# Performance work log

Hardware: AMD Instinct MI355X
Metric: run time of the kernel (lower is better)

Reference implementation:

```python
import jax, jax.numpy as jnp
import numpy as np

B, S, H, N_IN, N_PROC, R = 4, 1024, 1024, 64, 16, 128

def setup_inputs() -> dict:
    key = jax.random.key(0)
    k0, k1, k2, k3, k4 = jax.random.split(key, 5)
    intermediate = jax.random.normal(k0, (B, S, H), dtype=jnp.float32)
    enriched_activations = jax.random.normal(k1, (B, S, N_IN), dtype=jnp.float32)
    # Conv2d(1 -> N_proc, kernel=(5, N_in)), default PyTorch init scale ~ 1/sqrt(fan_in)
    fan_in = 1 * 5 * N_IN
    conv_w = jax.random.uniform(k2, (N_PROC, 1, 5, N_IN), dtype=jnp.float32,
                                minval=-1.0, maxval=1.0) / np.sqrt(fan_in).astype(np.float32)
    conv_b = jnp.zeros((N_PROC,), dtype=jnp.float32)
    down_proj = 0.02 * jax.random.normal(k3, (N_PROC, H, R), dtype=jnp.float32)
    up_proj = 0.02 * jax.random.normal(k4, (N_PROC, R, H), dtype=jnp.float32)
    return {"intermediate": intermediate, "enriched_activations": enriched_activations,
            "conv_w": conv_w, "conv_b": conv_b, "down_proj": down_proj, "up_proj": up_proj}

def reference(intermediate, enriched_activations, conv_w, conv_b, down_proj, up_proj):
    # act_map: [B, 1, S, N_in]; conv kernel (5, N_in) with padding (2, 0) -> [B, N_proc, S, 1]
    act_map = enriched_activations[:, None, :, :]
    pr = jax.lax.conv_general_dilated(
        act_map, conv_w, window_strides=(1, 1), padding=((2, 2), (0, 0)),
        dimension_numbers=("NCHW", "OIHW", "NCHW"))
    pr = pr + conv_b[None, :, None, None]
    # squeeze width, transpose to [B, S, N_proc], sigmoid gate
    process_activations = jax.nn.sigmoid(jnp.transpose(pr[..., 0], (0, 2, 1)))
    # per-expert low-rank transform
    down = jnp.einsum("bsh,nhr->bsnr", intermediate, down_proj)          # [B,S,N,R]
    transformed = jnp.einsum("bsnr,nrh->bsnh", down, up_proj)            # [B,S,N,H]
    # gate-weighted sum over experts (fuses multiply + sum over n)
    output = jnp.einsum("bsnh,bsn->bsh", transformed, process_activations)
    return (output, process_activations)
```

## Files before the change

### kernel.cpp

```cpp
#include <hip/hip_runtime.h>
#include <hip/hip_fp16.h>

#define T_TOK 4096
#define H_DIM 1024
#define NIN   64
#define NP    16
#define R_DIM 128
#define S_DIM 1024
#define N1    (NP * R_DIM)

typedef _Float16 half8  __attribute__((ext_vector_type(8)));
typedef _Float16 half4v __attribute__((ext_vector_type(4)));
typedef float    floatx16 __attribute__((ext_vector_type(16)));

typedef __attribute__((address_space(3))) unsigned char lds_u8_t;
typedef __attribute__((address_space(1))) unsigned char gbl_u8_t;

__device__ __forceinline__ void g2l16(const void* g, void* l) {
  __builtin_amdgcn_global_load_lds((const gbl_u8_t*)g, (lds_u8_t*)l, 16, 0, 0);
}

template <int GATE, int K, int N>
__global__ __launch_bounds__(256)
void gemm_kernel(const _Float16* __restrict__ A, const _Float16* __restrict__ BT,
                 const float* __restrict__ gv, void* __restrict__ Cv) {
  constexpr int NK = K / 64;
  constexpr int GX = N / 128;
  __shared__ __align__(16) _Float16 smem[4][64 * 128];

  const int tid = threadIdx.x, wave = tid >> 6, lane = tid & 63;
  const int id = blockIdx.x;
  const int xcd = id & 7, s = id >> 3;
  const int byi = s / GX + 4 * xcd;
  const int bxi = s % GX;
  const int m0 = byi * 128, n0 = bxi * 128;
  const int wr = (wave >> 1) * 64, wc = (wave & 1) * 64;
  const int rl = lane >> 4, ql = lane & 15;
  const int r = lane & 31, kh = lane >> 5;

  auto stage = [&](const _Float16* __restrict__ base, int off0, int k0,
                   _Float16* dst) {
    #pragma unroll
    for (int c = 0; c < 4; ++c) {
      const int cc = wave * 4 + c;
      const int lrow = cc * 4 + rl;
      const int cl = ql ^ (lrow & 15);
      const int row = lrow + ((cl >> 3) << 6);
      g2l16(base + (size_t)(off0 + row) * K + k0 + (cl & 7) * 8, dst + cc * 512);
    }
  };

  floatx16 acc[2][2];
  #pragma unroll
  for (int i = 0; i < 2; ++i)
    #pragma unroll
    for (int j = 0; j < 2; ++j) acc[i][j] = (floatx16)0.f;

  _Float16 *cA = smem[0], *nA = smem[1], *cB = smem[2], *nB = smem[3];
  stage(A, m0, 0, cA);
  stage(BT, n0, 0, cB);

  #pragma unroll 2
  for (int k = 0; k < NK; ++k) {
    if (k + 1 < NK) {
      stage(A, m0, (k + 1) * 64, nA);
      stage(BT, n0, (k + 1) * 64, nB);
      __builtin_amdgcn_s_waitcnt(0xF78);
    } else {
      __builtin_amdgcn_s_waitcnt(0xF70);
    }
    __builtin_amdgcn_s_barrier();
    __builtin_amdgcn_sched_barrier(0);
    #pragma unroll
    for (int h = 0; h < 4; ++h) {
      const int pA = (2 * h + kh + ((wave >> 1) << 3)) ^ (r & 15);
      const int pB = (2 * h + kh + ((wave & 1) << 3)) ^ (r & 15);
      half8 af[2], bf[2];
      #pragma unroll
      for (int i = 0; i < 2; ++i)
        af[i] = *reinterpret_cast<const half8*>(&cA[(i * 32 + r) * 128 + pA * 8]);
      #pragma unroll
      for (int j = 0; j < 2; ++j)
        bf[j] = *reinterpret_cast<const half8*>(&cB[(j * 32 + r) * 128 + pB * 8]);
      #pragma unroll
      for (int i = 0; i < 2; ++i)
        #pragma unroll
        for (int j = 0; j < 2; ++j)
          acc[i][j] = __builtin_amdgcn_mfma_f32_32x32x16_f16(af[i], bf[j], acc[i][j], 0, 0, 0);
    }
    __builtin_amdgcn_sched_barrier(0);
    __builtin_amdgcn_s_barrier();
    _Float16* t;
    t = cA; cA = nA; nA = t;
    t = cB; cB = nB; nB = t;
  }

  if (GATE) {
    _Float16* C = (_Float16*)Cv;
    #pragma unroll
    for (int i = 0; i < 2; ++i)
      #pragma unroll
      for (int g4 = 0; g4 < 4; ++g4)
        #pragma unroll
        for (int rr = 0; rr < 4; ++rr) {
          const int rowL = wr + i * 32 + rr + 8 * g4 + 4 * kh;
          const float g = gv[(size_t)(m0 + rowL) * NP + bxi];
          #pragma unroll
          for (int j = 0; j < 2; ++j)
            C[(size_t)(m0 + rowL) * N + n0 + wc + j * 32 + r] =
                (_Float16)(acc[i][j][g4 * 4 + rr] * g);
        }
  } else {
    float* C = (float*)Cv;
    #pragma unroll
    for (int i = 0; i < 2; ++i)
      #pragma unroll
      for (int g4 = 0; g4 < 4; ++g4)
        #pragma unroll
        for (int rr = 0; rr < 4; ++rr) {
          const int rowL = wr + i * 32 + rr + 8 * g4 + 4 * kh;
          #pragma unroll
          for (int j = 0; j < 2; ++j)
            C[(size_t)(m0 + rowL) * N + n0 + wc + j * 32 + r] = acc[i][j][g4 * 4 + rr];
        }
  }
}

__global__ __launch_bounds__(256)
void prep_kernel(const float* __restrict__ enr, const float* __restrict__ cw,
                 const float* __restrict__ cb, const float* __restrict__ inter,
                 const float* __restrict__ dproj, const float* __restrict__ uproj,
                 float* __restrict__ gates, _Float16* __restrict__ Xh,
                 _Float16* __restrict__ BT1, _Float16* __restrict__ UT) {
  __shared__ __align__(16) char smem[25664];
  const int tid = threadIdx.x;
  const int bx = blockIdx.x, nb = gridDim.x;
  {
    const float4* src = (const float4*)inter;
    half4v* dst = (half4v*)Xh;
    for (int i = bx * 256 + tid; i < T_TOK * H_DIM / 4; i += nb * 256) {
      float4 v = src[i];
      half4v o;
      o[0] = (_Float16)v.x; o[1] = (_Float16)v.y; o[2] = (_Float16)v.z; o[3] = (_Float16)v.w;
      dst[i] = o;
    }
  }
  if (bx < 256) {
    float (*sw)[321] = (float (*)[321])smem;
    float (*se)[NIN] = (float (*)[NIN])(smem + 20544);
    const int t0 = bx * 16;
    const int b = t0 >> 10, s0 = t0 & 1023;
    for (int i = tid; i < NP * 320; i += 256) sw[i / 320][i % 320] = cw[i];
    for (int i = tid; i < 20 * NIN; i += 256) {
      int rr = i >> 6, c = i & 63, s = s0 + rr - 2;
      se[rr][c] = (s >= 0 && s < S_DIM) ? enr[((size_t)b * S_DIM + s) * NIN + c] : 0.f;
    }
    __syncthreads();
    const int lt = tid >> 4, n = tid & 15;
    float acc = cb[n];
    #pragma unroll
    for (int dh = 0; dh < 5; ++dh) {
      const float* wrow = &sw[n][dh * 64];
      const float* erow = se[lt + dh];
      #pragma unroll
      for (int j = 0; j < NIN; ++j) acc += erow[j] * wrow[j];
    }
    gates[(size_t)(t0 + lt) * NP + n] = 1.f / (1.f + expf(-acc));
    __syncthreads();
  }
  for (int u = bx; u < 4096; u += nb) {
    const float* src; _Float16* dst; int rows, cols, bxt, byt;
    if (u < 2048) {
      int n = u >> 7, rem = u & 127;
      src = dproj + (size_t)n * H_DIM * R_DIM;
      dst = BT1 + (size_t)n * R_DIM * H_DIM;
      rows = H_DIM; cols = R_DIM; bxt = rem & 3; byt = rem >> 2;
    } else {
      int u2 = u - 2048;
      src = uproj; dst = UT; rows = N1; cols = H_DIM;
      bxt = u2 & 31; byt = u2 >> 5;
    }
    float (*tile)[33] = (float (*)[33])smem;
    const int c0 = bxt * 32, r0 = byt * 32;
    const int tx = tid & 31, ty = tid >> 5;
    #pragma unroll
    for (int k = 0; k < 32; k += 8)
      tile[ty + k][tx] = src[(size_t)(r0 + ty + k) * cols + c0 + tx];
    __syncthreads();
    #pragma unroll
    for (int k = 0; k < 32; k += 8)
      dst[(size_t)(c0 + ty + k) * rows + r0 + tx] = (_Float16)tile[tx][ty + k];
    __syncthreads();
  }
}

extern "C" void kernel_launch(void* const* d_in, const int* in_sizes, int n_in,
                              void* d_out, int out_size, void* d_ws, size_t ws_size,
                              hipStream_t stream) {
  const float* inter = (const float*)d_in[0];
  const float* enr   = (const float*)d_in[1];
  const float* convw = (const float*)d_in[2];
  const float* convb = (const float*)d_in[3];
  const float* dproj = (const float*)d_in[4];
  const float* uproj = (const float*)d_in[5];
  float* out   = (float*)d_out;
  float* gates = out + (size_t)T_TOK * H_DIM;

  _Float16* Xh  = (_Float16*)d_ws;
  _Float16* BT1 = Xh  + (size_t)T_TOK * H_DIM;
  _Float16* UT  = BT1 + (size_t)N1 * H_DIM;
  _Float16* Dsc = UT  + (size_t)H_DIM * N1;

  prep_kernel<<<8448, 256, 0, stream>>>(enr, convw, convb, inter, dproj, uproj,
                                        gates, Xh, BT1, UT);
  gemm_kernel<1, H_DIM, N1>
      <<<(N1 / 128) * (T_TOK / 128), 256, 0, stream>>>(Xh, BT1, gates, (void*)Dsc);
  gemm_kernel<0, N1, H_DIM>
      <<<(H_DIM / 128) * (T_TOK / 128), 256, 0, stream>>>(Dsc, UT, nullptr, (void*)out);
}
```

Measured before the change: 133.1 us.

## Fuse both GEMMs into one launch with per-row-block flag synchronization

Merges the down-projection and up-projection GEMMs into a single kernel of 768 blocks. The first 512 blocks compute gated Dsc tiles and atomically bump a per-row-block counter. The last 256 blocks spin on that counter until all 16 column tiles of their row block are written, then run the second GEMM. This removes a kernel launch boundary and lets the second GEMM start on finished row blocks while the first is still running. It relies on block scheduling order to avoid deadlock, and spinning blocks hold CUs while they wait.

```diff
diff --git a/kernel.cpp b/kernel.cpp
--- a/kernel.cpp
+++ b/kernel.cpp
@@ -21,15 +21,14 @@
 }
 
 template <int GATE, int K, int N>
-__global__ __launch_bounds__(256)
-void gemm_kernel(const _Float16* __restrict__ A, const _Float16* __restrict__ BT,
-                 const float* __restrict__ gv, void* __restrict__ Cv) {
+__device__ __forceinline__
+void gemm_body(_Float16* __restrict__ smem,
+               const _Float16* __restrict__ A, const _Float16* __restrict__ BT,
+               const float* __restrict__ gv, void* __restrict__ Cv,
+               int id, int tid, int* byi_out) {
   constexpr int NK = K / 64;
   constexpr int GX = N / 128;
-  __shared__ __align__(16) _Float16 smem[4][64 * 128];
-
-  const int tid = threadIdx.x, wave = tid >> 6, lane = tid & 63;
-  const int id = blockIdx.x;
+  const int wave = tid >> 6, lane = tid & 63;
   const int xcd = id & 7, s = id >> 3;
   const int byi = s / GX + 4 * xcd;
   const int bxi = s % GX;
@@ -37,6 +36,7 @@
   const int wr = (wave >> 1) * 64, wc = (wave & 1) * 64;
   const int rl = lane >> 4, ql = lane & 15;
   const int r = lane & 31, kh = lane >> 5;
+  *byi_out = byi;
 
   auto stage = [&](const _Float16* __restrict__ base, int off0, int k0,
                    _Float16* dst) {
@@ -56,7 +56,7 @@
     #pragma unroll
     for (int j = 0; j < 2; ++j) acc[i][j] = (floatx16)0.f;
 
-  _Float16 *cA = smem[0], *nA = smem[1], *cB = smem[2], *nB = smem[3];
+  _Float16 *cA = smem, *nA = smem + 8192, *cB = smem + 16384, *nB = smem + 24576;
   stage(A, m0, 0, cA);
   stage(BT, n0, 0, cB);
 
@@ -127,14 +127,51 @@
 }
 
 __global__ __launch_bounds__(256)
+void gemm_fused(const _Float16* __restrict__ Xh, const _Float16* __restrict__ BT1,
+                const _Float16* __restrict__ Dsc_c, _Float16* __restrict__ Dsc,
+                const _Float16* __restrict__ UT, const float* __restrict__ gates,
+                float* __restrict__ out, int* __restrict__ flags) {
+  __shared__ __align__(16) _Float16 smem[4 * 64 * 128];
+  const int tid = threadIdx.x;
+  const int bid = blockIdx.x;
+  int byi;
+  if (bid < 512) {
+    gemm_body<1, H_DIM, N1>(smem, Xh, BT1, gates, (void*)Dsc, bid, tid, &byi);
+    __syncthreads();
+    if (tid == 0) {
+      __threadfence();
+      __hip_atomic_fetch_add(&flags[byi], 1, __ATOMIC_RELEASE,
+                             __HIP_MEMORY_SCOPE_AGENT);
+    }
+  } else {
+    const int id = bid - 512;
+    {
+      const int xcd = id & 7, s = id >> 3;
+      byi = s / (H_DIM / 128) + 4 * xcd;
+    }
+    if (tid == 0) {
+      while (__hip_atomic_load(&flags[byi], __ATOMIC_ACQUIRE,
+                               __HIP_MEMORY_SCOPE_AGENT) < 16)
+        __builtin_amdgcn_s_sleep(8);
+      __threadfence();
+    }
+    __syncthreads();
+    int dummy;
+    gemm_body<0, N1, H_DIM>(smem, Dsc_c, UT, nullptr, (void*)out, id, tid, &dummy);
+  }
+}
+
+__global__ __launch_bounds__(256)
 void prep_kernel(const float* __restrict__ enr, const float* __restrict__ cw,
                  const float* __restrict__ cb, const float* __restrict__ inter,
                  const float* __restrict__ dproj, const float* __restrict__ uproj,
                  float* __restrict__ gates, _Float16* __restrict__ Xh,
-                 _Float16* __restrict__ BT1, _Float16* __restrict__ UT) {
+                 _Float16* __restrict__ BT1, _Float16* __restrict__ UT,
+                 int* __restrict__ flags) {
   __shared__ __align__(16) char smem[25664];
   const int tid = threadIdx.x;
   const int bx = blockIdx.x, nb = gridDim.x;
+  if (bx == 0 && tid < 32) flags[tid] = 0;
   {
     const float4* src = (const float4*)inter;
     half4v* dst = (half4v*)Xh;
@@ -210,11 +247,9 @@
   _Float16* BT1 = Xh  + (size_t)T_TOK * H_DIM;
   _Float16* UT  = BT1 + (size_t)N1 * H_DIM;
   _Float16* Dsc = UT  + (size_t)H_DIM * N1;
+  int* flags    = (int*)(Dsc + (size_t)T_TOK * N1);
 
   prep_kernel<<<8448, 256, 0, stream>>>(enr, convw, convb, inter, dproj, uproj,
-                                        gates, Xh, BT1, UT);
-  gemm_kernel<1, H_DIM, N1>
-      <<<(N1 / 128) * (T_TOK / 128), 256, 0, stream>>>(Xh, BT1, gates, (void*)Dsc);
-  gemm_kernel<0, N1, H_DIM>
-      <<<(H_DIM / 128) * (T_TOK / 128), 256, 0, stream>>>(Dsc, UT, nullptr, (void*)out);
-}
+                                        gates, Xh, BT1, UT, flags);
+  gemm_fused<<<768, 256, 0, stream>>>(Xh, BT1, Dsc, Dsc, UT, gates, out, flags);
+}
```

After: 192.5 us. 1.45x slower.
